# Performance work log

Measured on AMD Instinct MI355X. Metric: run time of the kernel, lower is better.

## Reference

```python
import jax, jax.numpy as jnp
import numpy as np

B, N, M = 4, 1024, 4096
DQ, DC = 1024, 1024
H, DH = 16, 64
INNER = H * DH
SCALE = DH ** -0.5


def setup_inputs() -> dict:
    key = jax.random.key(0)
    ks = jax.random.split(key, 6)
    x = jax.random.normal(ks[0], (B, N, DQ), dtype=jnp.float32)
    context = jax.random.normal(ks[1], (B, M, DC), dtype=jnp.float32)
    mask = jax.random.bernoulli(ks[2], 0.9, (B, M))  # bool, True = keep
    # weights, scaled like default torch Linear init (~1/sqrt(fan_in))
    Wq = jax.random.normal(ks[3], (DQ, INNER), dtype=jnp.float32) / np.sqrt(DQ)
    Wkv = jax.random.normal(ks[4], (DC, 2 * INNER), dtype=jnp.float32) / np.sqrt(DC)
    Wo = jax.random.normal(ks[5], (INNER, DQ), dtype=jnp.float32) / np.sqrt(INNER)
    bo = jnp.zeros((DQ,), dtype=jnp.float32)
    return {"x": x, "context": context, "mask": mask,
            "Wq": Wq, "Wkv": Wkv, "Wo": Wo, "bo": bo}


def reference(x, context, mask, Wq, Wkv, Wo, bo):
    # projections
    q = x @ Wq                     # [b, n, h*d]
    kv = context @ Wkv             # [b, m, 2*h*d]
    k, v = jnp.split(kv, 2, axis=-1)
    # split heads: [b, s, h*d] -> [b, h, s, d]
    def heads(t):
        b, s, _ = t.shape
        return t.reshape(b, s, H, DH).transpose(0, 2, 1, 3)
    q, k, v = heads(q), heads(k), heads(v)
    sim = jnp.einsum('bhid,bhjd->bhij', q, k) * SCALE   # [b, h, n, m]
    max_neg = -jnp.finfo(sim.dtype).max
    sim = jnp.where(mask[:, None, None, :], sim, max_neg)
    sim = jnp.clip(sim, -5.0, 5.0)  # masked entries become exactly -5
    attn = jax.nn.softmax(sim, axis=-1)
    out = jnp.einsum('bhij,bhjd->bhid', attn, v)        # [b, h, n, d]
    out = out.transpose(0, 2, 1, 3).reshape(x.shape[0], x.shape[1], INNER)
    return out @ Wo + bo
```

## Files before the change

kernel.cpp:

```cpp
#include <hip/hip_runtime.h>
#include <hip/hip_bf16.h>


typedef __attribute__((ext_vector_type(8))) short short8;
typedef __attribute__((ext_vector_type(8))) unsigned short u16x8;
typedef __attribute__((ext_vector_type(4))) float f32x4;
typedef __attribute__((ext_vector_type(16))) float f32x16;

static __device__ __forceinline__ void gload_lds16(const void* g, void* l) {
  __builtin_amdgcn_global_load_lds((const __attribute__((address_space(1))) void*)g,
                                   (__attribute__((address_space(3))) void*)l, 16, 0, 0);
}

static __device__ __forceinline__ unsigned short f2bf(float f) {
  __hip_bfloat16 h = __float2bfloat16(f);
  unsigned short u;
  __builtin_memcpy(&u, &h, 2);
  return u;
}

static __device__ __forceinline__ float bf2f(unsigned short u) {
  unsigned int x = (unsigned int)u << 16;
  float f;
  __builtin_memcpy(&f, &x, 4);
  return f;
}

static __device__ __forceinline__ unsigned int pack_rnd(float a, float b) {
  unsigned int ua, ub;
  __builtin_memcpy(&ua, &a, 4);
  __builtin_memcpy(&ub, &b, 4);
  return __builtin_amdgcn_perm(ua + 0x8000u, ub + 0x8000u, 0x03020706u);
}

__global__ __launch_bounds__(256) void cast_bf16_kernel(const float* __restrict__ in,
                                                        unsigned short* __restrict__ out,
                                                        int n8) {
  int idx = blockIdx.x * 256 + threadIdx.x;
  int stride = gridDim.x * 256;
  for (int i = idx; i < n8; i += stride) {
    const float4* p = (const float4*)in + (size_t)i * 2;
    float4 a = p[0], b = p[1];
    u16x8 r;
    r[0] = f2bf(a.x); r[1] = f2bf(a.y); r[2] = f2bf(a.z); r[3] = f2bf(a.w);
    r[4] = f2bf(b.x); r[5] = f2bf(b.y); r[6] = f2bf(b.z); r[7] = f2bf(b.w);
    *((u16x8*)out + i) = r;
  }
}

__global__ __launch_bounds__(256) void mask_bias_kernel(const int* __restrict__ mask,
                                                        float* __restrict__ bias, int n) {
  int i = blockIdx.x * 256 + threadIdx.x;
  if (i < n) bias[i] = mask[i] ? 0.0f : -1e30f;
}

__global__ __launch_bounds__(256) void transpose_cast_kernel(const float* __restrict__ W,
                                                             unsigned short* __restrict__ Wt,
                                                             int K, int N) {
  __shared__ float tile[32][33];
  int n0 = blockIdx.x * 32, k0 = blockIdx.y * 32;
  int tx = threadIdx.x & 31, ty = threadIdx.x >> 5;
#pragma unroll
  for (int r = 0; r < 32; r += 8)
    tile[ty + r][tx] = W[(size_t)(k0 + ty + r) * N + n0 + tx];
  __syncthreads();
#pragma unroll
  for (int r = 0; r < 32; r += 8)
    Wt[(size_t)(n0 + ty + r) * K + k0 + tx] = f2bf(tile[tx][ty + r]);
}

template <int EPI>
__global__ __launch_bounds__(256, 2) void gemm_bt_kernel(
    const unsigned short* __restrict__ A, const unsigned short* __restrict__ Bt,
    int M, int N, int K,
    unsigned short* __restrict__ out0, unsigned short* __restrict__ out1,
    float* __restrict__ outF, const float* __restrict__ bias) {
  __shared__ unsigned short As[128 * 64];
  __shared__ unsigned short Bs[128 * 64];
  const int tid = threadIdx.x;
  const int l = tid & 63;
  const int lq = l & 15, g = l >> 4;
  const int w = tid >> 6;
  const int wr = w >> 1, wc = w & 1;
  const int nwg = gridDim.x * gridDim.y;
  const int idl = blockIdx.y * gridDim.x + blockIdx.x;
  const int lin = (idl & 7) * (nwg >> 3) + (idl >> 3);
  const int m0 = (lin / gridDim.x) * 128, n0 = (lin % gridDim.x) * 128;

  f32x4 acc[4][4] = {};

  for (int k0 = 0; k0 < K; k0 += 64) {
    __syncthreads();
#pragma unroll
    for (int t = 0; t < 4; ++t) {
      int c = t * 256 + tid;
      int row = c >> 3, cb = c & 7;
      int srcoff = (cb * 16) ^ ((row & 7) << 4);
      char* la = (char*)As + t * 4096 + (tid & 192) * 16;
      gload_lds16((const char*)(A + (size_t)(m0 + row) * K + k0) + srcoff, la);
      char* lb = (char*)Bs + t * 4096 + (tid & 192) * 16;
      gload_lds16((const char*)(Bt + (size_t)(n0 + row) * K + k0) + srcoff, lb);
    }
    __syncthreads();
#pragma unroll
    for (int ks = 0; ks < 2; ++ks) {
      short8 af[4], bfr[4];
#pragma unroll
      for (int mt = 0; mt < 4; ++mt) {
        int row = wr * 64 + mt * 16 + lq;
        af[mt] = *(const short8*)&As[row * 64 + ((ks * 32 + g * 8) ^ ((row & 7) << 3))];
      }
#pragma unroll
      for (int nt = 0; nt < 4; ++nt) {
        int row = wc * 64 + nt * 16 + lq;
        bfr[nt] = *(const short8*)&Bs[row * 64 + ((ks * 32 + g * 8) ^ ((row & 7) << 3))];
      }
#pragma unroll
      for (int mt = 0; mt < 4; ++mt)
#pragma unroll
        for (int nt = 0; nt < 4; ++nt)
          acc[mt][nt] =
              __builtin_amdgcn_mfma_f32_16x16x32_bf16(af[mt], bfr[nt], acc[mt][nt], 0, 0, 0);
    }
  }

#pragma unroll
  for (int mt = 0; mt < 4; ++mt) {
#pragma unroll
    for (int nt = 0; nt < 4; ++nt) {
      if (EPI == 1 && n0 >= 1024) {
        int colb = n0 - 1024 + wc * 64 + nt * 16 + lq;
        int h = colb >> 6, d = colb & 63;
        int rowb = m0 + wr * 64 + mt * 16 + g * 4;
        int b = rowb >> 12, mm = rowb & 4095;
        ushort4 pk;
        pk.x = f2bf(acc[mt][nt][0]);
        pk.y = f2bf(acc[mt][nt][1]);
        pk.z = f2bf(acc[mt][nt][2]);
        pk.w = f2bf(acc[mt][nt][3]);
        size_t off = (((size_t)(b * 16 + h) * 512 + (mm >> 3)) * 64 + d) * 8 + (mm & 7);
        *(ushort4*)&out1[off] = pk;
      } else {
#pragma unroll
        for (int r = 0; r < 4; ++r) {
          int row = m0 + wr * 64 + mt * 16 + g * 4 + r;
          int col = n0 + wc * 64 + nt * 16 + lq;
          float v = acc[mt][nt][r];
          if (EPI == 0) {
            int b = row >> 10, nq = row & 1023;
            int h = col >> 6, d = col & 63;
            out0[(((size_t)(b * 16 + h)) * 1024 + nq) * 64 + d] =
                f2bf(v * 0.18033688011112042f);
          } else if (EPI == 1) {
            int b = row >> 12, mm = row & 4095;
            int h = col >> 6, d = col & 63;
            size_t off = (((size_t)(b * 16 + h) * 8 + (d >> 3)) * 4096 + mm) * 8 + (d & 7);
            out0[off] = f2bf(v);
          } else {
            outF[(size_t)row * 1024 + col] = v + bias[col];
          }
        }
      }
    }
  }
}

__global__ __launch_bounds__(256, 3) void attn_kernel(
    const unsigned short* __restrict__ K2, const unsigned short* __restrict__ V2,
    const unsigned short* __restrict__ Q, const float* __restrict__ maskb,
    unsigned short* __restrict__ numP, float* __restrict__ denP) {
  __shared__ unsigned short Ks[2][8 * 64 * 8];
  __shared__ unsigned short Vt[2][8 * 64 * 8];

  const int tid = threadIdx.x;
  const int l = tid & 63, w = tid >> 6;
  const int lq = l & 31;
  const int hi = l >> 5;

  const int id = blockIdx.x;
  const int xcd = id & 7;
  const int kk = id >> 3;
  const int qi = kk & 7;
  const int pr = xcd * 32 + (kk >> 3);
  const int bh = pr & 63, js = pr >> 6;
  const int b = bh >> 4;
  const int q0 = qi * 128 + w * 32;

  const unsigned short* Qh = Q + (size_t)bh * 1024 * 64;
  const unsigned short* Kh = K2 + (size_t)bh * 8 * 4096 * 8;
  const unsigned short* Vh = V2 + (size_t)bh * 512 * 64 * 8;
  const float* bb = maskb + b * 4096;

  const float CLIP2 = 7.213475204444817f;

  short8 qf[4];
#pragma unroll
  for (int kc = 0; kc < 4; ++kc)
    qf[kc] = *(const short8*)&Qh[(size_t)(q0 + lq) * 64 + kc * 16 + hi * 8];

  f32x16 oacc[2] = {};
  float den = 0.f;

  const int jbeg = js * 16, jend = jbeg + 16;

#define STAGE_KV(bi_, j0_)                                                       \
  do {                                                                           \
    _Pragma("unroll") for (int t = 0; t < 2; ++t) {                              \
      int c = t * 256 + tid;                                                     \
      int db = c >> 6, jj = c & 63;                                              \
      int sig = (jj & 0x33) | ((jj & 4) << 1) | ((jj & 8) >> 1);                 \
      char* lk = (char*)(&Ks[bi_][0]) + t * 4096 + (tid & 192) * 16;             \
      gload_lds16((const char*)(Kh + ((size_t)db * 4096 + (j0_) + sig) * 8), lk);\
      char* lv = (char*)(&Vt[bi_][0]) + t * 4096 + (tid & 192) * 16;             \
      gload_lds16((const char*)(Vh + ((size_t)(((j0_) >> 3) + db) * 64 + jj) * 8), lv); \
    }                                                                            \
  } while (0)

  STAGE_KV(0, jbeg * 64);
  __syncthreads();

  for (int jt = jbeg; jt < jend; ++jt) {
    const int j0 = jt * 64;
    const int cur = jt & 1;
    if (jt + 1 < jend) STAGE_KV(cur ^ 1, j0 + 64);

    const unsigned short* Kc = &Ks[cur][0];
    const unsigned short* Vc = &Vt[cur][0];

#pragma unroll
    for (int half = 0; half < 2; ++half) {
      f32x16 sacc;
#pragma unroll
      for (int bq = 0; bq < 4; ++bq) {
        f32x4 m4 = *(const f32x4*)&bb[j0 + half * 32 + ((bq & 1) << 2) + (hi << 3) +
                                      ((bq >> 1) << 4)];
        sacc[bq * 4 + 0] = m4[0];
        sacc[bq * 4 + 1] = m4[1];
        sacc[bq * 4 + 2] = m4[2];
        sacc[bq * 4 + 3] = m4[3];
      }
      __builtin_amdgcn_s_setprio(1);
#pragma unroll
      for (int kc = 0; kc < 4; ++kc) {
        short8 kf = *(const short8*)((const char*)Kc + (2 * kc + hi) * 1024 +
                                     (half * 32 + lq) * 16);
        sacc = __builtin_amdgcn_mfma_f32_32x32x16_bf16(kf, qf[kc], sacc, 0, 0, 0);
      }
      __builtin_amdgcn_s_setprio(0);
#pragma unroll
      for (int r = 0; r < 16; ++r) {
        float v = __builtin_amdgcn_fmed3f(sacc[r], -CLIP2, CLIP2);
        float p = __builtin_amdgcn_exp2f(v);
        sacc[r] = p;
        den += p;
      }
      unsigned int wds[8];
#pragma unroll
      for (int i = 0; i < 8; ++i) wds[i] = pack_rnd(sacc[i * 2], sacc[i * 2 + 1]);
      __builtin_amdgcn_s_setprio(1);
#pragma unroll
      for (int kt = 0; kt < 2; ++kt) {
        union { unsigned int u[4]; short8 s; } pa;
        pa.u[0] = wds[kt * 4 + 0];
        pa.u[1] = wds[kt * 4 + 1];
        pa.u[2] = wds[kt * 4 + 2];
        pa.u[3] = wds[kt * 4 + 3];
#pragma unroll
        for (int dt = 0; dt < 2; ++dt) {
          short8 vf = *(const short8*)((const char*)Vc +
              (4 * half + 2 * kt + hi) * 1024 + (dt * 32 + lq) * 16);
          oacc[dt] = __builtin_amdgcn_mfma_f32_32x32x16_bf16(pa.s, vf, oacc[dt], 0, 0, 0);
        }
      }
      __builtin_amdgcn_s_setprio(0);
    }
    __syncthreads();
  }
#undef STAGE_KV

  den += __shfl_xor(den, 32);
  if (l < 32) denP[(((size_t)js * 64 + bh) * 1024) + q0 + l] = den;

#pragma unroll
  for (int dt = 0; dt < 2; ++dt)
#pragma unroll
    for (int r = 0; r < 16; ++r) {
      int q = q0 + (r & 3) + 8 * (r >> 2) + 4 * hi;
      int d = dt * 32 + lq;
      numP[((((size_t)js * 64 + bh) * 1024 + q) * 64) + d] = f2bf(oacc[dt][r]);
    }
}

__global__ __launch_bounds__(256) void attn_reduce_kernel(
    const unsigned short* __restrict__ numP, const float* __restrict__ denP,
    unsigned short* __restrict__ Ob) {
  int id = blockIdx.x * 256 + threadIdx.x;
  int d8 = id & 7;
  int q = (id >> 3) & 1023;
  int bh = id >> 13;
  int b = bh >> 4, h = bh & 15;
  float den = 0.f;
  float o[8] = {0.f, 0.f, 0.f, 0.f, 0.f, 0.f, 0.f, 0.f};
#pragma unroll
  for (int s = 0; s < 4; ++s) {
    const unsigned short* np =
        numP + ((((size_t)s * 64 + bh) * 1024 + q) * 64 + d8 * 8);
    u16x8 v = *(const u16x8*)np;
    den += denP[((size_t)s * 64 + bh) * 1024 + q];
#pragma unroll
    for (int e = 0; e < 8; ++e) o[e] += bf2f(v[e]);
  }
  float r = 1.0f / den;
  u16x8 outv;
#pragma unroll
  for (int e = 0; e < 8; ++e) outv[e] = f2bf(o[e] * r);
  *(u16x8*)&Ob[(((size_t)b * 1024 + q) * 1024) + h * 64 + d8 * 8] = outv;
}

extern "C" void kernel_launch(void* const* d_in, const int* in_sizes, int n_in,
                              void* d_out, int out_size, void* d_ws, size_t ws_size,
                              hipStream_t stream) {
  (void)in_sizes; (void)n_in; (void)out_size; (void)ws_size;
  const float* x    = (const float*)d_in[0];
  const float* ctx  = (const float*)d_in[1];
  const int*   mask = (const int*)d_in[2];
  const float* Wq   = (const float*)d_in[3];
  const float* Wkv  = (const float*)d_in[4];
  const float* Wo   = (const float*)d_in[5];
  const float* bo   = (const float*)d_in[6];
  float* out = (float*)d_out;

  char* ws = (char*)d_ws;
  const size_t MB = 1 << 20;
  unsigned short* numP = (unsigned short*)(ws + 0);
  float*          denP = (float*)(ws + 32 * MB);
  float*          mbias= (float*)(ws + 33 * MB);
  unsigned short* xb   = (unsigned short*)(ws + 0);
  unsigned short* cb   = (unsigned short*)(ws + 8 * MB);
  unsigned short* WqT  = (unsigned short*)(ws + 40 * MB);
  unsigned short* WkvT = (unsigned short*)(ws + 42 * MB);
  unsigned short* WoT  = (unsigned short*)(ws + 46 * MB);
  unsigned short* Qb   = (unsigned short*)(ws + 48 * MB);
  unsigned short* K2   = (unsigned short*)(ws + 56 * MB);
  unsigned short* V2   = (unsigned short*)(ws + 88 * MB);
  unsigned short* Ob   = (unsigned short*)(ws + 120 * MB);

  cast_bf16_kernel<<<2048, 256, 0, stream>>>(x, xb, (4 * 1024 * 1024) / 8);
  cast_bf16_kernel<<<2048, 256, 0, stream>>>(ctx, cb, (16 * 1024 * 1024) / 8);
  transpose_cast_kernel<<<dim3(32, 32), 256, 0, stream>>>(Wq, WqT, 1024, 1024);
  transpose_cast_kernel<<<dim3(64, 32), 256, 0, stream>>>(Wkv, WkvT, 1024, 2048);
  transpose_cast_kernel<<<dim3(32, 32), 256, 0, stream>>>(Wo, WoT, 1024, 1024);

  gemm_bt_kernel<0><<<dim3(8, 32), 256, 0, stream>>>(xb, WqT, 4096, 1024, 1024,
                                                     Qb, (unsigned short*)nullptr,
                                                     (float*)nullptr, (const float*)nullptr);
  gemm_bt_kernel<1><<<dim3(16, 128), 256, 0, stream>>>(cb, WkvT, 16384, 2048, 1024,
                                                       K2, V2,
                                                       (float*)nullptr, (const float*)nullptr);
  mask_bias_kernel<<<64, 256, 0, stream>>>(mask, mbias, 4 * 4096);
  attn_kernel<<<2048, 256, 0, stream>>>(K2, V2, Qb, mbias, numP, denP);
  attn_reduce_kernel<<<2048, 256, 0, stream>>>(numP, denP, Ob);
  gemm_bt_kernel<2><<<dim3(8, 32), 256, 0, stream>>>(Ob, WoT, 4096, 1024, 1024,
                                                     (unsigned short*)nullptr, (unsigned short*)nullptr,
                                                     out, bo);
}
```

Before: 243.2 us.

## Add dedicated 256x256-tile 4-stage pipelined GEMM for KV projection

Replaces the generic 128x128 GEMM used for the context KV projection with a specialized kernel using 256x256 tiles, 512 threads, and a 4-deep LDS ring fed by direct global-to-LDS loads with explicit waitcnt and barrier scheduling. It also raises MFMA priority during compute. The larger tiles and deeper prefetch aim to improve data reuse and hide memory latency on the largest GEMM. In exchange it uses much more LDS per block, hardcodes K=1024, and the K output is written as scattered 2-byte stores.

```diff
diff --git a/kernel.cpp b/kernel.cpp
--- a/kernel.cpp
+++ b/kernel.cpp
@@ -73,7 +73,7 @@
 __global__ __launch_bounds__(256, 2) void gemm_bt_kernel(
     const unsigned short* __restrict__ A, const unsigned short* __restrict__ Bt,
     int M, int N, int K,
-    unsigned short* __restrict__ out0, unsigned short* __restrict__ out1,
+    unsigned short* __restrict__ out0,
     float* __restrict__ outF, const float* __restrict__ bias) {
   __shared__ unsigned short As[128 * 64];
   __shared__ unsigned short Bs[128 * 64];
@@ -128,38 +128,133 @@
   for (int mt = 0; mt < 4; ++mt) {
 #pragma unroll
     for (int nt = 0; nt < 4; ++nt) {
-      if (EPI == 1 && n0 >= 1024) {
-        int colb = n0 - 1024 + wc * 64 + nt * 16 + lq;
-        int h = colb >> 6, d = colb & 63;
-        int rowb = m0 + wr * 64 + mt * 16 + g * 4;
-        int b = rowb >> 12, mm = rowb & 4095;
+#pragma unroll
+      for (int r = 0; r < 4; ++r) {
+        int row = m0 + wr * 64 + mt * 16 + g * 4 + r;
+        int col = n0 + wc * 64 + nt * 16 + lq;
+        float v = acc[mt][nt][r];
+        if (EPI == 0) {
+          int b = row >> 10, nq = row & 1023;
+          int h = col >> 6, d = col & 63;
+          out0[(((size_t)(b * 16 + h)) * 1024 + nq) * 64 + d] =
+              f2bf(v * 0.18033688011112042f);
+        } else {
+          outF[(size_t)row * 1024 + col] = v + bias[col];
+        }
+      }
+    }
+  }
+}
+
+__global__ __launch_bounds__(512, 2) void gemm256_kv_kernel(
+    const unsigned short* __restrict__ A, const unsigned short* __restrict__ Bt,
+    unsigned short* __restrict__ K2out, unsigned short* __restrict__ V2out) {
+  __shared__ unsigned short lds[4 * 16384];
+  const int tid = threadIdx.x;
+  const int l = tid & 63;
+  const int lq = l & 15, g = l >> 4;
+  const int w = tid >> 6;
+  const int wr = w >> 2, wc = w & 3;
+  const int nwg = gridDim.x * gridDim.y;
+  const int idl = blockIdx.y * gridDim.x + blockIdx.x;
+  const int lin = (idl & 7) * (nwg >> 3) + (idl >> 3);
+  const int m0 = (lin / gridDim.x) * 256;
+  const int n0 = (lin % gridDim.x) * 256;
+
+  const int rA0 = tid >> 2, rA1 = (512 + tid) >> 2;
+  const int ch = tid & 3;
+  const unsigned short* sA0 = A + (size_t)(m0 + rA0) * 1024 + ((ch ^ (rA0 & 3)) << 3);
+  const unsigned short* sA1 = A + (size_t)(m0 + rA1) * 1024 + ((ch ^ (rA1 & 3)) << 3);
+  const unsigned short* sB0 = Bt + (size_t)(n0 + rA0) * 1024 + ((ch ^ (rA0 & 3)) << 3);
+  const unsigned short* sB1 = Bt + (size_t)(n0 + rA1) * 1024 + ((ch ^ (rA1 & 3)) << 3);
+  const int wub = (tid & 448) * 16;
+
+  const int coff = (g ^ (lq & 3)) << 4;
+  const int aoff = (wr * 128 + lq) * 64 + coff;
+  const int boff = 16384 + (wc * 64 + lq) * 64 + coff;
+
+  f32x4 acc[8][4] = {};
+
+#define STAGE256(t_, s_)                                                   \
+  do {                                                                     \
+    char* _b = (char*)lds + (s_) * 32768;                                  \
+    gload_lds16(sA0 + (t_) * 32, _b + wub);                                \
+    gload_lds16(sA1 + (t_) * 32, _b + 8192 + wub);                         \
+    gload_lds16(sB0 + (t_) * 32, _b + 16384 + wub);                        \
+    gload_lds16(sB1 + (t_) * 32, _b + 24576 + wub);                        \
+  } while (0)
+
+#define COMPUTE256(s_)                                                     \
+  do {                                                                     \
+    const char* _pa = (const char*)lds + (s_) * 32768 + aoff;              \
+    const char* _pb = (const char*)lds + (s_) * 32768 + boff;              \
+    short8 af[8], bfv[4];                                                  \
+    _Pragma("unroll") for (int mt = 0; mt < 8; ++mt)                       \
+        af[mt] = *(const short8*)(_pa + mt * 1024);                        \
+    _Pragma("unroll") for (int nt = 0; nt < 4; ++nt)                       \
+        bfv[nt] = *(const short8*)(_pb + nt * 1024);                       \
+    __builtin_amdgcn_s_setprio(1);                                         \
+    _Pragma("unroll") for (int mt = 0; mt < 8; ++mt)                       \
+        _Pragma("unroll") for (int nt = 0; nt < 4; ++nt)                   \
+            acc[mt][nt] = __builtin_amdgcn_mfma_f32_16x16x32_bf16(         \
+                af[mt], bfv[nt], acc[mt][nt], 0, 0, 0);                    \
+    __builtin_amdgcn_s_setprio(0);                                         \
+  } while (0)
+
+#define PHASE256(vm_, dostage_, t_, s_stage_, s_comp_)                     \
+  do {                                                                     \
+    asm volatile("s_waitcnt vmcnt(" #vm_ ")" ::: "memory");                \
+    __builtin_amdgcn_s_barrier();                                          \
+    __builtin_amdgcn_sched_barrier(0);                                     \
+    if (dostage_) STAGE256(t_, s_stage_);                                  \
+    COMPUTE256(s_comp_);                                                   \
+  } while (0)
+
+  STAGE256(0, 0);
+  STAGE256(1, 1);
+  STAGE256(2, 2);
+
+  for (int it = 0; it < 7; ++it) {
+    const int t0 = it * 4;
+    PHASE256(8, true, t0 + 3, 3, 0);
+    PHASE256(8, true, t0 + 4, 0, 1);
+    PHASE256(8, true, t0 + 5, 1, 2);
+    PHASE256(8, true, t0 + 6, 2, 3);
+  }
+  PHASE256(8, true, 31, 3, 0);
+  PHASE256(8, false, 0, 0, 1);
+  PHASE256(4, false, 0, 0, 2);
+  PHASE256(0, false, 0, 0, 3);
+
+#undef PHASE256
+#undef COMPUTE256
+#undef STAGE256
+
+#pragma unroll
+  for (int mt = 0; mt < 8; ++mt) {
+#pragma unroll
+    for (int nt = 0; nt < 4; ++nt) {
+      int col = n0 + wc * 64 + nt * 16 + lq;
+      int rowb = m0 + wr * 128 + mt * 16 + g * 4;
+      int b = rowb >> 12, mm = rowb & 4095;
+      if (col < 1024) {
+        int h = col >> 6, d = col & 63;
+#pragma unroll
+        for (int r = 0; r < 4; ++r) {
+          size_t off =
+              (((size_t)(b * 16 + h) * 8 + (d >> 3)) * 4096 + (mm + r)) * 8 + (d & 7);
+          K2out[off] = f2bf(acc[mt][nt][r]);
+        }
+      } else {
+        int hv = col - 1024;
+        int h = hv >> 6, d = hv & 63;
         ushort4 pk;
         pk.x = f2bf(acc[mt][nt][0]);
         pk.y = f2bf(acc[mt][nt][1]);
         pk.z = f2bf(acc[mt][nt][2]);
         pk.w = f2bf(acc[mt][nt][3]);
         size_t off = (((size_t)(b * 16 + h) * 512 + (mm >> 3)) * 64 + d) * 8 + (mm & 7);
-        *(ushort4*)&out1[off] = pk;
-      } else {
-#pragma unroll
-        for (int r = 0; r < 4; ++r) {
-          int row = m0 + wr * 64 + mt * 16 + g * 4 + r;
-          int col = n0 + wc * 64 + nt * 16 + lq;
-          float v = acc[mt][nt][r];
-          if (EPI == 0) {
-            int b = row >> 10, nq = row & 1023;
-            int h = col >> 6, d = col & 63;
-            out0[(((size_t)(b * 16 + h)) * 1024 + nq) * 64 + d] =
-                f2bf(v * 0.18033688011112042f);
-          } else if (EPI == 1) {
-            int b = row >> 12, mm = row & 4095;
-            int h = col >> 6, d = col & 63;
-            size_t off = (((size_t)(b * 16 + h) * 8 + (d >> 3)) * 4096 + mm) * 8 + (d & 7);
-            out0[off] = f2bf(v);
-          } else {
-            outF[(size_t)row * 1024 + col] = v + bias[col];
-          }
-        }
+        *(ushort4*)&V2out[off] = pk;
       }
     }
   }
@@ -352,15 +447,13 @@
   transpose_cast_kernel<<<dim3(32, 32), 256, 0, stream>>>(Wo, WoT, 1024, 1024);
 
   gemm_bt_kernel<0><<<dim3(8, 32), 256, 0, stream>>>(xb, WqT, 4096, 1024, 1024,
-                                                     Qb, (unsigned short*)nullptr,
-                                                     (float*)nullptr, (const float*)nullptr);
-  gemm_bt_kernel<1><<<dim3(16, 128), 256, 0, stream>>>(cb, WkvT, 16384, 2048, 1024,
-                                                       K2, V2,
-                                                       (float*)nullptr, (const float*)nullptr);
+                                                     Qb, (float*)nullptr,
+                                                     (const float*)nullptr);
+  gemm256_kv_kernel<<<dim3(8, 64), 512, 0, stream>>>(cb, WkvT, K2, V2);
   mask_bias_kernel<<<64, 256, 0, stream>>>(mask, mbias, 4 * 4096);
   attn_kernel<<<2048, 256, 0, stream>>>(K2, V2, Qb, mbias, numP, denP);
   attn_reduce_kernel<<<2048, 256, 0, stream>>>(numP, denP, Ob);
   gemm_bt_kernel<2><<<dim3(8, 32), 256, 0, stream>>>(Ob, WoT, 4096, 1024, 1024,
-                                                     (unsigned short*)nullptr, (unsigned short*)nullptr,
+                                                     (unsigned short*)nullptr,
                                                      out, bo);
 }
```

Result: no change. 244.8 us (+0.7%).
